# Kernel tuning notes

Measured on AMD Instinct MI355X. Metric: run time of the kernel, lower is better.

The kernel has to match this reference:

```python
import jax, jax.numpy as jnp
import numpy as np
from jax import lax

B, H, W = 2, 128, 128
DIM, HEADS, WS, SHIFT = 192, 6, 16, 8
NT, RD, CS, HID, K = 128, 20, 256, 384, 5
N = H * W
HD = DIM // HEADS


def _rpi(ws):
    coords = np.stack(np.meshgrid(np.arange(ws), np.arange(ws), indexing='ij')).reshape(2, -1)
    rel = (coords[:, :, None] - coords[:, None, :]).transpose(1, 2, 0).astype(np.int64)
    rel[:, :, 0] += ws - 1
    rel[:, :, 1] += ws - 1
    rel[:, :, 0] *= 2 * ws - 1
    return rel.sum(-1)


def _attn_mask(h, w, ws, shift):
    img = np.zeros((h, w))
    cnt = 0
    for hs in (slice(0, -ws), slice(-ws, -shift), slice(-shift, None)):
        for wsl in (slice(0, -ws), slice(-ws, -shift), slice(-shift, None)):
            img[hs, wsl] = cnt
            cnt += 1
    mw = img.reshape(h // ws, ws, w // ws, ws).transpose(0, 2, 1, 3).reshape(-1, ws * ws)
    am = mw[:, None, :] - mw[:, :, None]
    return np.where(am != 0, -100.0, 0.0).astype(np.float32)


def setup_inputs():
    key = jax.random.key(0)
    ks = jax.random.split(key, 16)
    f32 = jnp.float32
    rn = lambda k, shp, s=0.02: jax.random.normal(k, shp, dtype=f32) * s
    return {
        'x': jax.random.normal(ks[0], (B, N, DIM), dtype=f32),
        'td': jax.random.normal(ks[1], (B, NT, DIM), dtype=f32),
        'attn_mask': jnp.asarray(_attn_mask(H, W, WS, SHIFT)),
        'wqkv_w': rn(ks[2], (DIM, 3 * DIM)), 'wqkv_b': jnp.zeros((3 * DIM,), f32),
        'rpb_table': rn(ks[3], ((2 * WS - 1) ** 2, HEADS)),
        'win_proj_w': rn(ks[4], (DIM, DIM)), 'win_proj_b': jnp.zeros((DIM,), f32),
        'wq_w': rn(ks[5], (DIM, RD)), 'wq_b': jnp.zeros((RD,), f32),
        'wk_w': rn(ks[6], (DIM, RD)), 'wk_b': jnp.zeros((RD,), f32),
        'wv_w': rn(ks[7], (DIM, DIM)), 'wv_b': jnp.zeros((DIM,), f32),
        'atd_scale': jnp.full((NT,), 0.5, f32),
        'aca_proj_w': rn(ks[8], (DIM, DIM)), 'aca_proj_b': jnp.zeros((DIM,), f32),
        'logit_scale': jnp.full((1, 1), float(np.log(10.0)), f32),
        'fc1_w': rn(ks[9], (DIM, HID)), 'fc1_b': jnp.zeros((HID,), f32),
        'dw_w': rn(ks[10], (HID, 1, K, K)), 'dw_b': jnp.zeros((HID,), f32),
        'fc2_w': rn(ks[11], (HID, DIM)), 'fc2_b': jnp.zeros((DIM,), f32),
        'ln1_w': jnp.ones((DIM,), f32), 'ln1_b': jnp.zeros((DIM,), f32),
        'ln2_w': jnp.ones((DIM,), f32), 'ln2_b': jnp.zeros((DIM,), f32),
        'in3_w': jnp.ones((NT,), f32), 'in3_b': jnp.zeros((NT,), f32),
        'sigma': jnp.zeros((NT, 1), f32),
        'rpi': jnp.asarray(_rpi(WS)),
        'h': H, 'w': W,
    }


def _ln(x, w, b, eps=1e-5):
    mu = x.mean(-1, keepdims=True)
    var = ((x - mu) ** 2).mean(-1, keepdims=True)
    return (x - mu) * lax.rsqrt(var + eps) * w + b


def reference(x, td, attn_mask, wqkv_w, wqkv_b, rpb_table, win_proj_w, win_proj_b,
              wq_w, wq_b, wk_w, wk_b, wv_w, wv_b, atd_scale, aca_proj_w, aca_proj_b,
              logit_scale, fc1_w, fc1_b, dw_w, dw_b, fc2_w, fc2_b,
              ln1_w, ln1_b, ln2_w, ln2_b, in3_w, in3_b, sigma, rpi, h, w):
    b, n, c = x.shape
    shortcut = x
    xn = _ln(x, ln1_w, ln1_b)
    qkv = xn @ wqkv_w + wqkv_b  # (b, n, 3c)

    # ---- shifted-window MSA ----
    g = jnp.roll(qkv.reshape(b, h, w, 3 * c), (-SHIFT, -SHIFT), axis=(1, 2))
    nwh, nww = h // WS, w // WS
    nw2 = WS * WS
    win = g.reshape(b, nwh, WS, nww, WS, 3 * c).transpose(0, 1, 3, 2, 4, 5)
    win = win.reshape(b * nwh * nww, nw2, 3, HEADS, HD)
    q, k, v = (win[:, :, i].transpose(0, 2, 1, 3) for i in range(3))  # (b_, H, nw2, hd)
    attn = jnp.einsum('bhid,bhjd->bhij', q * (HD ** -0.5), k)
    rpb = rpb_table[rpi.reshape(-1)].reshape(nw2, nw2, HEADS).transpose(2, 0, 1)
    nwin = nwh * nww
    attn = attn.reshape(b, nwin, HEADS, nw2, nw2) + rpb[None, None] + attn_mask[None, :, None]
    attn = jax.nn.softmax(attn, axis=-1).reshape(-1, HEADS, nw2, nw2)
    o = jnp.einsum('bhij,bhjd->bhid', attn, v).transpose(0, 2, 1, 3).reshape(-1, nw2, c)
    o = o @ win_proj_w + win_proj_b
    o = o.reshape(b, nwh, nww, WS, WS, c).transpose(0, 1, 3, 2, 4, 5).reshape(b, h, w, c)
    x_win = jnp.roll(o, (SHIFT, SHIFT), axis=(1, 2)).reshape(b, n, c)

    # ---- adaptive token dictionary cross-attention ----
    qa = xn @ wq_w + wq_b
    ka = td @ wk_w + wk_b
    va = td @ wv_w + wv_b
    qa = qa / jnp.maximum(jnp.linalg.norm(qa, axis=-1, keepdims=True), 1e-12)
    ka = ka / jnp.maximum(jnp.linalg.norm(ka, axis=-1, keepdims=True), 1e-12)
    s = jnp.clip(atd_scale, 0.0, 1.0)
    sim = jax.nn.softmax(jnp.einsum('bnr,btr->bnt', qa, ka) * (1.0 + s * float(np.log(NT))), axis=-1)
    x_atd = jnp.einsum('bnt,btc->bnc', sim, va)

    # ---- adaptive category MSA (sort-gather-attend-scatter) ----
    gs = min(n, CS)
    ng = (n + gs - 1) // gs
    pad_n = ng * gs - n
    tk_id = jnp.argmax(sim, axis=-1)                      # (b, n)
    sort_idx = jnp.argsort(tk_id, axis=-1)
    inv_idx = jnp.argsort(sort_idx, axis=-1)              # inverse permutation
    shuf = jnp.take_along_axis(qkv, sort_idx[:, :, None], axis=1)
    if pad_n > 0:
        shuf = jnp.concatenate([shuf, shuf[:, n - pad_n:n][:, ::-1]], axis=1)
    y = shuf.reshape(b, ng, gs, 3, HEADS, HD)
    qg, kg, vg = (y[:, :, :, i].transpose(0, 1, 3, 2, 4) for i in range(3))  # (b, ng, H, gs, hd)
    ls = jnp.exp(jnp.minimum(logit_scale, float(np.log(100.0))))[0, 0]
    ag = jax.nn.softmax(jnp.einsum('bghid,bghjd->bghij', qg, kg) * ls, axis=-1)
    og = jnp.einsum('bghij,bghjd->bghid', ag, vg).transpose(0, 1, 3, 2, 4).reshape(b, ng * gs, c)[:, :n]
    og = jnp.take_along_axis(og, inv_idx[:, :, None], axis=1)
    x_aca = og @ aca_proj_w + aca_proj_b

    x = shortcut + x_win + x_atd + x_aca

    # ---- ConvFFN ----
    xn2 = _ln(x, ln2_w, ln2_b)
    hdn = jax.nn.gelu(xn2 @ fc1_w + fc1_b, approximate=False)
    grid = hdn.transpose(0, 2, 1).reshape(b, HID, h, w)
    grid = lax.conv_general_dilated(grid, dw_w, (1, 1), [(K // 2, K // 2)] * 2,
                                    feature_group_count=HID)
    grid = jax.nn.gelu(grid + dw_b[None, :, None, None], approximate=False)
    x = x + (grid.reshape(b, HID, n).transpose(0, 2, 1) @ fc2_w + fc2_b)

    # ---- token dictionary refinement ----
    mask_soft = jax.nn.softmax(jnp.swapaxes(sim, -1, -2), axis=-1)  # (b, NT, n)
    td_new = sigma * td + (1.0 - sigma) * jnp.einsum('btn,bnc->btc', mask_soft, x)
    mu = td_new.mean(-1, keepdims=True)
    var = ((td_new - mu) ** 2).mean(-1, keepdims=True)
    td_new = (td_new - mu) * lax.rsqrt(var + 1e-5) * in3_w[None, :, None] + in3_b[None, :, None]

    return x, td_new
```

## Files before the change

kernel.cpp:

```cpp
#include <hip/hip_runtime.h>
#include <math.h>

#define NB    2
#define HH    128
#define WW2   128
#define NN    16384
#define DIM_  192
#define HEADS_ 6
#define HD_   32
#define NT_   128
#define RD_   20
#define HID_  384
#define ROWS  32768
#define HD_SCALE 0.17677669529663687f
#define LOG100   4.6051701859880914f
#define LOGNT    4.852030263919617f

__device__ __forceinline__ float gelu_f(float v) {
  return 0.5f * v * (1.0f + erff(v * 0.7071067811865475f));
}

__device__ __forceinline__ int winmap_row(int r) {
  int b_ = r >> 8;
  int p  = r & 255;
  int b  = b_ >> 6;
  int win = b_ & 63;
  int y = ((win >> 3) << 4) + (p >> 4);
  int x = ((win & 7) << 4) + (p & 15);
  int n = (((y + 8) & 127) << 7) + ((x + 8) & 127);
  return (b << 14) + n;
}

__device__ __forceinline__ int rgn(int v) { return (v >= 112 ? 1 : 0) + (v >= 120 ? 1 : 0); }

__global__ __launch_bounds__(256)
void ln_kernel(const float* __restrict__ in, const float* __restrict__ w,
               const float* __restrict__ bv, float* __restrict__ out, int nrows) {
  int wave = threadIdx.x >> 6, lane = threadIdx.x & 63;
  int row = blockIdx.x * 4 + wave;
  if (row >= nrows) return;
  const float* p = in + (size_t)row * DIM_;
  float v0 = p[lane], v1 = p[lane + 64], v2 = p[lane + 128];
  float s = v0 + v1 + v2;
  #pragma unroll
  for (int m = 32; m; m >>= 1) s += __shfl_xor(s, m, 64);
  float mu = s * (1.0f / 192.0f);
  float d0 = v0 - mu, d1 = v1 - mu, d2 = v2 - mu;
  float q = d0 * d0 + d1 * d1 + d2 * d2;
  #pragma unroll
  for (int m = 32; m; m >>= 1) q += __shfl_xor(q, m, 64);
  float rs = rsqrtf(q * (1.0f / 192.0f) + 1e-5f);
  float* o = out + (size_t)row * DIM_;
  o[lane]       = d0 * rs * w[lane]       + bv[lane];
  o[lane + 64]  = d1 * rs * w[lane + 64]  + bv[lane + 64];
  o[lane + 128] = d2 * rs * w[lane + 128] + bv[lane + 128];
}

template<bool AT, bool BIAS, bool DOGELU, int RMODE, bool ADD>
__global__ __launch_bounds__(256)
void gemm128(const float* __restrict__ A, const float* __restrict__ W,
             const float* __restrict__ bias, float* __restrict__ C,
             int M, int N, int K, int lda, const int* __restrict__ rowmap) {
  __shared__ float As[32][128];
  __shared__ float Bs[32][64];
  int tid = threadIdx.x;
  int tx = tid & 15, ty = tid >> 4;
  int m0 = blockIdx.y * 128, n0 = blockIdx.x * 64;
  float acc[8][4] = {};
  for (int k0 = 0; k0 < K; k0 += 32) {
    if (!AT) {
      #pragma unroll
      for (int q = 0; q < 4; ++q) {
        int i = tid * 4 + q;
        int r = i >> 3, c4 = (i & 7) << 2;
        float4 v = *(const float4*)(A + (size_t)(m0 + r) * lda + k0 + c4);
        As[c4 + 0][r] = v.x; As[c4 + 1][r] = v.y; As[c4 + 2][r] = v.z; As[c4 + 3][r] = v.w;
      }
    } else {
      #pragma unroll
      for (int q = 0; q < 4; ++q) {
        int i = q * 256 + tid;
        int kc = i >> 5, mr4 = (i & 31) << 2;
        float4 v = *(const float4*)(A + (size_t)(k0 + kc) * lda + m0 + mr4);
        *(float4*)&As[kc][mr4] = v;
      }
    }
    #pragma unroll
    for (int q = 0; q < 2; ++q) {
      int i = tid * 2 + q;
      int kc = i >> 4, nc = (i & 15) << 2;
      int col = n0 + nc;
      float4 v = make_float4(0.f, 0.f, 0.f, 0.f);
      if (col + 3 < N) {
        v = *(const float4*)(W + (size_t)(k0 + kc) * N + col);
      } else {
        float t[4] = {0.f, 0.f, 0.f, 0.f};
        #pragma unroll
        for (int e = 0; e < 4; ++e) if (col + e < N) t[e] = W[(size_t)(k0 + kc) * N + col + e];
        v = make_float4(t[0], t[1], t[2], t[3]);
      }
      *(float4*)&Bs[kc][nc] = v;
    }
    __syncthreads();
    #pragma unroll
    for (int kk = 0; kk < 32; ++kk) {
      float4 a0 = *(const float4*)&As[kk][ty * 8];
      float4 a1 = *(const float4*)&As[kk][ty * 8 + 4];
      float4 b  = *(const float4*)&Bs[kk][tx * 4];
      float av[8] = {a0.x, a0.y, a0.z, a0.w, a1.x, a1.y, a1.z, a1.w};
      #pragma unroll
      for (int ii = 0; ii < 8; ++ii) {
        acc[ii][0] += av[ii] * b.x; acc[ii][1] += av[ii] * b.y;
        acc[ii][2] += av[ii] * b.z; acc[ii][3] += av[ii] * b.w;
      }
    }
    __syncthreads();
  }
  #pragma unroll
  for (int ii = 0; ii < 8; ++ii) {
    int row = m0 + ty * 8 + ii;
    int drow;
    if (RMODE == 1) drow = winmap_row(row);
    else if (RMODE == 2) drow = rowmap[row];
    else drow = row;
    float* crow = C + (size_t)drow * N;
    #pragma unroll
    for (int j = 0; j < 4; ++j) {
      int col = n0 + tx * 4 + j;
      if (col < N) {
        float v = acc[ii][j];
        if (BIAS) v += bias[col];
        if (DOGELU) v = gelu_f(v);
        if (ADD) crow[col] += v; else crow[col] = v;
      }
    }
  }
}

__global__ __launch_bounds__(256)
void attn2_kernel(const float* __restrict__ qkv, const int* __restrict__ sort_row,
                  const float* __restrict__ rpb_table, const float* __restrict__ ls_ptr,
                  float* __restrict__ obufW, float* __restrict__ obufC) {
  __shared__ float Ks[128][32];
  __shared__ float Vs[128][32];
  __shared__ float rpb_s[964];
  int b_ = blockIdx.x, head = blockIdx.y;
  bool IS_WIN = (blockIdx.z == 0);
  int tid = threadIdx.x;

  if (IS_WIN) {
    for (int idx = tid; idx < 961; idx += 256) rpb_s[idx] = rpb_table[idx * HEADS_ + head];
  }

  int gq = b_ * 256 + tid;
  int srcq = IS_WIN ? winmap_row(gq) : sort_row[gq];
  float qr[32];
  {
    const float4* rowp = (const float4*)(qkv + (size_t)srcq * 576);
    #pragma unroll
    for (int q4 = 0; q4 < 8; ++q4) {
      float4 v = rowp[head * 8 + q4];
      qr[q4 * 4] = v.x; qr[q4 * 4 + 1] = v.y; qr[q4 * 4 + 2] = v.z; qr[q4 * 4 + 3] = v.w;
    }
  }
  float scale = IS_WIN ? HD_SCALE : __expf(fminf(ls_ptr[0], LOG100));

  int win = b_ & 63;
  int wy = (win >> 3) << 4, wx = (win & 7) << 4;
  int py = tid >> 4, px = tid & 15;
  int ri = rgn(wy + py) * 3 + rgn(wx + px);

  float m = -3.4e38f, l = 0.f, acc[32];
  #pragma unroll
  for (int d = 0; d < 32; ++d) acc[d] = 0.f;

  for (int c0 = 0; c0 < 256; c0 += 128) {
    __syncthreads();
    #pragma unroll
    for (int it = 0; it < 4; ++it) {
      int j = it * 32 + (tid >> 3);
      int q4 = tid & 7;
      int src = IS_WIN ? winmap_row(b_ * 256 + c0 + j) : sort_row[b_ * 256 + c0 + j];
      const float4* rowp = (const float4*)(qkv + (size_t)src * 576);
      *(float4*)&Ks[j][q4 << 2] = rowp[48 + head * 8 + q4];
      *(float4*)&Vs[j][q4 << 2] = rowp[96 + head * 8 + q4];
    }
    __syncthreads();

    for (int j0 = 0; j0 < 128; j0 += 16) {
      float s[16];
      #pragma unroll
      for (int jj = 0; jj < 16; ++jj) {
        const float* kp = Ks[j0 + jj];
        float4 k0v = *(const float4*)(kp + 0),  k1v = *(const float4*)(kp + 4);
        float4 k2v = *(const float4*)(kp + 8),  k3v = *(const float4*)(kp + 12);
        float4 k4v = *(const float4*)(kp + 16), k5v = *(const float4*)(kp + 20);
        float4 k6v = *(const float4*)(kp + 24), k7v = *(const float4*)(kp + 28);
        float a = qr[0]*k0v.x + qr[1]*k0v.y + qr[2]*k0v.z + qr[3]*k0v.w
                + qr[4]*k1v.x + qr[5]*k1v.y + qr[6]*k1v.z + qr[7]*k1v.w
                + qr[8]*k2v.x + qr[9]*k2v.y + qr[10]*k2v.z + qr[11]*k2v.w
                + qr[12]*k3v.x + qr[13]*k3v.y + qr[14]*k3v.z + qr[15]*k3v.w
                + qr[16]*k4v.x + qr[17]*k4v.y + qr[18]*k4v.z + qr[19]*k4v.w
                + qr[20]*k5v.x + qr[21]*k5v.y + qr[22]*k5v.z + qr[23]*k5v.w
                + qr[24]*k6v.x + qr[25]*k6v.y + qr[26]*k6v.z + qr[27]*k6v.w
                + qr[28]*k7v.x + qr[29]*k7v.y + qr[30]*k7v.z + qr[31]*k7v.w;
        a *= scale;
        if (IS_WIN) {
          int jab = c0 + j0 + jj;
          int jy = jab >> 4, jx = jab & 15;
          int idx = (py - jy + 15) * 31 + (px - jx + 15);
          int rj = rgn(wy + jy) * 3 + rgn(wx + jx);
          a += rpb_s[idx] + (ri != rj ? -100.0f : 0.0f);
        }
        s[jj] = a;
      }
      float cm = s[0];
      #pragma unroll
      for (int jj = 1; jj < 16; ++jj) cm = fmaxf(cm, s[jj]);
      float mn = fmaxf(m, cm);
      float corr = __expf(m - mn);
      l *= corr;
      #pragma unroll
      for (int d = 0; d < 32; ++d) acc[d] *= corr;
      #pragma unroll
      for (int jj = 0; jj < 16; ++jj) {
        float p = __expf(s[jj] - mn);
        l += p;
        const float* vp = Vs[j0 + jj];
        #pragma unroll
        for (int d = 0; d < 32; ++d) acc[d] += p * vp[d];
      }
      m = mn;
    }
  }
  float inv = 1.0f / l;
  float* obuf = IS_WIN ? obufW : obufC;
  float* op = obuf + ((size_t)(b_ * 256 + tid)) * DIM_ + head * HD_;
  #pragma unroll
  for (int d4 = 0; d4 < 8; ++d4) {
    float4 v = make_float4(acc[d4 * 4] * inv, acc[d4 * 4 + 1] * inv,
                           acc[d4 * 4 + 2] * inv, acc[d4 * 4 + 3] * inv);
    *(float4*)(op + d4 * 4) = v;
  }
}

__global__ __launch_bounds__(256)
void normrows20(float* __restrict__ p, int rows) {
  int r = blockIdx.x * 256 + threadIdx.x;
  if (r >= rows) return;
  float4* rp = (float4*)(p + (size_t)r * RD_);
  float4 v[5];
  float s = 0.f;
  #pragma unroll
  for (int e = 0; e < 5; ++e) {
    v[e] = rp[e];
    s += v[e].x * v[e].x + v[e].y * v[e].y + v[e].z * v[e].z + v[e].w * v[e].w;
  }
  float inv = 1.0f / fmaxf(sqrtf(s), 1e-12f);
  #pragma unroll
  for (int e = 0; e < 5; ++e) {
    v[e].x *= inv; v[e].y *= inv; v[e].z *= inv; v[e].w *= inv;
    rp[e] = v[e];
  }
}

__global__ __launch_bounds__(256)
void sim1_kernel(const float* __restrict__ qa, const float* __restrict__ ka,
                 const float* __restrict__ atd_scale, float* __restrict__ simT,
                 float* __restrict__ m_out, float* __restrict__ den_out, int* __restrict__ tk) {
  __shared__ float kas[NT_ * RD_];
  __shared__ float scl[NT_];
  int tid = threadIdx.x;
  int gi = blockIdx.x * 256 + tid;
  int b = blockIdx.x >> 6;
  for (int idx = tid; idx < NT_ * RD_; idx += 256) kas[idx] = ka[b * NT_ * RD_ + idx];
  for (int t = tid; t < NT_; t += 256)
    scl[t] = 1.0f + fminf(fmaxf(atd_scale[t], 0.f), 1.f) * LOGNT;
  __syncthreads();
  float q[20];
  const float4* qp = (const float4*)(qa + (size_t)gi * RD_);
  #pragma unroll
  for (int e = 0; e < 5; ++e) {
    float4 v = qp[e];
    q[e * 4] = v.x; q[e * 4 + 1] = v.y; q[e * 4 + 2] = v.z; q[e * 4 + 3] = v.w;
  }
  int n = gi & (NN - 1);
  float m = -3.4e38f, l = 0.f;
  int am = 0;
  float* srow = simT + (size_t)b * NT_ * NN + n;
  for (int t = 0; t < NT_; ++t) {
    const float* kp = &kas[t * RD_];
    float d = 0.f;
    #pragma unroll
    for (int e = 0; e < 20; ++e) d += q[e] * kp[e];
    d *= scl[t];
    srow[(size_t)t * NN] = d;
    if (d > m) { l = l * __expf(m - d) + 1.0f; m = d; am = t; }
    else       { l += __expf(d - m); }
  }
  m_out[gi] = m; den_out[gi] = l; tk[gi] = am;
}

__global__ __launch_bounds__(256)
void sim2_kernel(float* __restrict__ simT, const float* __restrict__ m_i,
                 const float* __restrict__ den_i) {
  size_t idx = (size_t)blockIdx.x * 256 + threadIdx.x;
  int b = (int)(idx >> 21);
  int n = (int)(idx & (NN - 1));
  int gi = (b << 14) + n;
  float r = simT[idx];
  simT[idx] = __expf(r - m_i[gi]) / den_i[gi];
}

__global__ __launch_bounds__(256)
void hist_kernel(const int* __restrict__ tk, int* __restrict__ chist) {
  __shared__ int h[NT_];
  int tid = threadIdx.x, ch = blockIdx.x, b = blockIdx.y;
  if (tid < NT_) h[tid] = 0;
  __syncthreads();
  int bin = tk[b * NN + ch * 256 + tid];
  atomicAdd(&h[bin], 1);
  __syncthreads();
  if (tid < NT_) chist[(b * 64 + ch) * NT_ + tid] = h[tid];
}

__global__ __launch_bounds__(128)
void offsets_kernel(const int* __restrict__ chist, int* __restrict__ offs) {
  int b = blockIdx.x, bin = threadIdx.x;
  int total = 0;
  for (int ch = 0; ch < 64; ++ch) total += chist[(b * 64 + ch) * NT_ + bin];
  __shared__ int sc[NT_];
  sc[bin] = total;
  __syncthreads();
  int base = 0;
  for (int i = 0; i < bin; ++i) base += sc[i];
  int run = base;
  for (int ch = 0; ch < 64; ++ch) {
    offs[(b * 64 + ch) * NT_ + bin] = run;
    run += chist[(b * 64 + ch) * NT_ + bin];
  }
}

__global__ __launch_bounds__(256)
void scatter_kernel(const int* __restrict__ tk, const int* __restrict__ offs,
                    int* __restrict__ sort_row) {
  __shared__ int bins[256];
  int tid = threadIdx.x, ch = blockIdx.x, b = blockIdx.y;
  int i = ch * 256 + tid;
  int bin = tk[b * NN + i];
  bins[tid] = bin;
  __syncthreads();
  int rank = 0;
  for (int j = 0; j < tid; ++j) rank += (bins[j] == bin) ? 1 : 0;
  int pos = offs[(b * 64 + ch) * NT_ + bin] + rank;
  sort_row[b * NN + pos] = b * NN + i;
}

__global__ __launch_bounds__(384)
void dwconv_kernel(const float* __restrict__ hdn, const float* __restrict__ wgt,
                   const float* __restrict__ bv, float* __restrict__ out) {
  int c = threadIdx.x;
  int xt = blockIdx.x, y = blockIdx.y, b = blockIdx.z;
  float wr[25];
  #pragma unroll
  for (int t = 0; t < 25; ++t) wr[t] = wgt[c * 25 + t];
  float bias = bv[c];
  int x0 = xt * 16;
  const float* base = hdn + (size_t)b * NN * HID_;
  float win[5][5];
  #pragma unroll
  for (int r = 0; r < 5; ++r) {
    int yy = y + r - 2;
    #pragma unroll
    for (int t = 0; t < 4; ++t) {
      int xx = x0 - 2 + t;
      win[r][t] = (yy >= 0 && yy < HH && xx >= 0 && xx < WW2)
                    ? base[((size_t)yy * WW2 + xx) * HID_ + c] : 0.f;
    }
  }
  for (int x = x0; x < x0 + 16; ++x) {
    int xx = x + 2;
    #pragma unroll
    for (int r = 0; r < 5; ++r) {
      int yy = y + r - 2;
      win[r][4] = (yy >= 0 && yy < HH && xx < WW2)
                    ? base[((size_t)yy * WW2 + xx) * HID_ + c] : 0.f;
    }
    float s = bias;
    #pragma unroll
    for (int r = 0; r < 5; ++r)
      #pragma unroll
      for (int t = 0; t < 5; ++t) s += win[r][t] * wr[r * 5 + t];
    s = gelu_f(s);
    out[((size_t)b * NN + (size_t)y * WW2 + x) * HID_ + c] = s;
    #pragma unroll
    for (int r = 0; r < 5; ++r) {
      win[r][0] = win[r][1]; win[r][1] = win[r][2];
      win[r][2] = win[r][3]; win[r][3] = win[r][4];
    }
  }
}

__global__ __launch_bounds__(256)
void tdstats_kernel(const float* __restrict__ simT, float* __restrict__ tmax,
                    float* __restrict__ tden) {
  int bt = blockIdx.x;
  int tid = threadIdx.x;
  const float* row = simT + (size_t)bt * NN;
  float m = -3.4e38f;
  for (int i = tid; i < NN; i += 256) m = fmaxf(m, row[i]);
  __shared__ float red[256];
  red[tid] = m;
  __syncthreads();
  for (int s = 128; s > 0; s >>= 1) {
    if (tid < s) red[tid] = fmaxf(red[tid], red[tid + s]);
    __syncthreads();
  }
  float mrow = red[0];
  __syncthreads();
  float ssum = 0.f;
  for (int i = tid; i < NN; i += 256) ssum += __expf(row[i] - mrow);
  red[tid] = ssum;
  __syncthreads();
  for (int s = 128; s > 0; s >>= 1) {
    if (tid < s) red[tid] += red[tid + s];
    __syncthreads();
  }
  if (tid == 0) { tmax[bt] = mrow; tden[bt] = red[0]; }
}

__global__ __launch_bounds__(192)
void tdgemm_kernel(const float* __restrict__ simT, const float* __restrict__ tmax,
                   const float* __restrict__ tden, const float* __restrict__ xf,
                   float* __restrict__ tdacc) {
  int nch = blockIdx.x, tt4 = blockIdx.y, b = blockIdx.z;
  int t0 = tt4 * 32;
  int n0 = nch * 512;
  __shared__ float wtile[32][64];
  float acc[32] = {};
  int tid = threadIdx.x;
  for (int sub = 0; sub < 8; ++sub) {
    int nb = n0 + sub * 64;
    __syncthreads();
    for (int idx = tid; idx < 2048; idx += 192) {
      int trow = idx >> 6, nn = idx & 63;
      int t = t0 + trow;
      float raw = simT[((size_t)(b * NT_ + t)) * NN + nb + nn];
      wtile[trow][nn] = __expf(raw - tmax[b * NT_ + t]) / tden[b * NT_ + t];
    }
    __syncthreads();
    for (int nn = 0; nn < 64; ++nn) {
      float xv = xf[((size_t)(b * NN + nb + nn)) * DIM_ + tid];
      #pragma unroll
      for (int trow = 0; trow < 32; ++trow) acc[trow] += wtile[trow][nn] * xv;
    }
  }
  #pragma unroll
  for (int trow = 0; trow < 32; ++trow)
    atomicAdd(&tdacc[((size_t)(b * NT_ + t0 + trow)) * DIM_ + tid], acc[trow]);
}

__global__ __launch_bounds__(64)
void tdfinal_kernel(const float* __restrict__ td, const float* __restrict__ tdacc,
                    const float* __restrict__ sigma, const float* __restrict__ in3w,
                    const float* __restrict__ in3b, float* __restrict__ out) {
  int r = blockIdx.x;
  int lane = threadIdx.x;
  int t = r & (NT_ - 1);
  float sg = sigma[t];
  const float* ta = tdacc + (size_t)r * DIM_;
  const float* tp = td + (size_t)r * DIM_;
  float v0 = sg * tp[lane]       + (1.f - sg) * ta[lane];
  float v1 = sg * tp[lane + 64]  + (1.f - sg) * ta[lane + 64];
  float v2 = sg * tp[lane + 128] + (1.f - sg) * ta[lane + 128];
  float s = v0 + v1 + v2;
  #pragma unroll
  for (int m = 32; m; m >>= 1) s += __shfl_xor(s, m, 64);
  float mu = s * (1.0f / 192.0f);
  float d0 = v0 - mu, d1 = v1 - mu, d2 = v2 - mu;
  float q = d0 * d0 + d1 * d1 + d2 * d2;
  #pragma unroll
// ... 15 lines not shown
  const float* wqkv_w     = (const float*)d_in[3];
  const float* wqkv_b     = (const float*)d_in[4];
  const float* rpb_table  = (const float*)d_in[5];
  const float* win_proj_w = (const float*)d_in[6];
  const float* win_proj_b = (const float*)d_in[7];
  const float* wq_w       = (const float*)d_in[8];
  const float* wq_b       = (const float*)d_in[9];
  const float* wk_w       = (const float*)d_in[10];
  const float* wk_b       = (const float*)d_in[11];
  const float* wv_w       = (const float*)d_in[12];
  const float* wv_b       = (const float*)d_in[13];
  const float* atd_scale  = (const float*)d_in[14];
  const float* aca_proj_w = (const float*)d_in[15];
  const float* aca_proj_b = (const float*)d_in[16];
  const float* logit_scale= (const float*)d_in[17];
  const float* fc1_w      = (const float*)d_in[18];
  const float* fc1_b      = (const float*)d_in[19];
  const float* dw_w       = (const float*)d_in[20];
  const float* dw_b       = (const float*)d_in[21];
  const float* fc2_w      = (const float*)d_in[22];
  const float* fc2_b      = (const float*)d_in[23];
  const float* ln1_w      = (const float*)d_in[24];
  const float* ln1_b      = (const float*)d_in[25];
  const float* ln2_w      = (const float*)d_in[26];
  const float* ln2_b      = (const float*)d_in[27];
  const float* in3_w      = (const float*)d_in[28];
  const float* in3_b      = (const float*)d_in[29];
  const float* sigma      = (const float*)d_in[30];

  float* out = (float*)d_out;

  float* wsf = (float*)d_ws;
  size_t o = 0;
  float* xn    = wsf + o; o += (size_t)ROWS * DIM_;
  float* qkv   = wsf + o; o += (size_t)ROWS * 3 * DIM_;
  float* obufW = wsf + o; o += (size_t)ROWS * DIM_;
  float* simT  = wsf + o; o += (size_t)NB * NT_ * NN;
  float* gridb = wsf + o; o += (size_t)ROWS * HID_;
  float* qa    = wsf + o; o += (size_t)ROWS * RD_;
  float* ka    = wsf + o; o += (size_t)NB * NT_ * RD_;
  float* va    = wsf + o; o += (size_t)NB * NT_ * DIM_;
  float* m_i   = wsf + o; o += ROWS;
  float* den_i = wsf + o; o += ROWS;
  float* tmaxb = wsf + o; o += NB * NT_;
  float* tdenb = wsf + o; o += NB * NT_;
  float* tdacc = wsf + o; o += (size_t)NB * NT_ * DIM_;
  int* tk      = (int*)(wsf + o); o += ROWS;
  int* chist   = (int*)(wsf + o); o += NB * 64 * NT_;
  int* coffs   = (int*)(wsf + o); o += NB * 64 * NT_;
  int* sort_row= (int*)(wsf + o); o += ROWS;
  float* hdn   = qkv;
  float* obufC = gridb;

  hipMemcpyAsync(out, x, (size_t)ROWS * DIM_ * sizeof(float),
                 hipMemcpyDeviceToDevice, stream);
  ln_kernel<<<ROWS / 4, 256, 0, stream>>>(x, ln1_w, ln1_b, xn, ROWS);
  gemm128<false, true, false, 0, false><<<dim3(9, ROWS / 128), 256, 0, stream>>>(
      xn, wqkv_w, wqkv_b, qkv, ROWS, 576, 192, 192, nullptr);
  gemm128<false, true, false, 0, false><<<dim3(1, ROWS / 128), 256, 0, stream>>>(
      xn, wq_w, wq_b, qa, ROWS, 20, 192, 192, nullptr);
  gemm128<false, true, false, 0, false><<<dim3(1, 2), 256, 0, stream>>>(
      td, wk_w, wk_b, ka, NB * NT_, 20, 192, 192, nullptr);
  gemm128<false, true, false, 0, false><<<dim3(3, 2), 256, 0, stream>>>(
      td, wv_w, wv_b, va, NB * NT_, 192, 192, 192, nullptr);
  normrows20<<<ROWS / 256, 256, 0, stream>>>(qa, ROWS);
  normrows20<<<1, 256, 0, stream>>>(ka, NB * NT_);
  sim1_kernel<<<ROWS / 256, 256, 0, stream>>>(qa, ka, atd_scale, simT, m_i, den_i, tk);
  sim2_kernel<<<(NB * NT_ * NN) / 256, 256, 0, stream>>>(simT, m_i, den_i);
  hist_kernel<<<dim3(64, NB), 256, 0, stream>>>(tk, chist);
  offsets_kernel<<<NB, 128, 0, stream>>>(chist, coffs);
  scatter_kernel<<<dim3(64, NB), 256, 0, stream>>>(tk, coffs, sort_row);
  attn2_kernel<<<dim3(128, 6, 2), 256, 0, stream>>>(
      qkv, sort_row, rpb_table, logit_scale, obufW, obufC);
  gemm128<false, true, false, 1, true><<<dim3(3, ROWS / 128), 256, 0, stream>>>(
      obufW, win_proj_w, win_proj_b, out, ROWS, 192, 192, 192, nullptr);
  gemm128<false, true, false, 2, true><<<dim3(3, ROWS / 128), 256, 0, stream>>>(
      obufC, aca_proj_w, aca_proj_b, out, ROWS, 192, 192, 192, sort_row);
  for (int b = 0; b < NB; ++b) {
    gemm128<true, false, false, 0, true><<<dim3(3, NN / 128), 256, 0, stream>>>(
        simT + (size_t)b * NT_ * NN, va + (size_t)b * NT_ * DIM_, nullptr,
        out + (size_t)b * NN * DIM_, NN, 192, 128, NN, nullptr);
  }
  ln_kernel<<<ROWS / 4, 256, 0, stream>>>(out, ln2_w, ln2_b, xn, ROWS);
  gemm128<false, true, true, 0, false><<<dim3(6, ROWS / 128), 256, 0, stream>>>(
      xn, fc1_w, fc1_b, hdn, ROWS, 384, 192, 192, nullptr);
  dwconv_kernel<<<dim3(8, 128, NB), 384, 0, stream>>>(hdn, dw_w, dw_b, gridb);
  gemm128<false, true, false, 0, true><<<dim3(3, ROWS / 128), 256, 0, stream>>>(
      gridb, fc2_w, fc2_b, out, ROWS, 192, 384, 384, nullptr);
  tdstats_kernel<<<NB * NT_, 256, 0, stream>>>(simT, tmaxb, tdenb);
  hipMemsetAsync(tdacc, 0, (size_t)NB * NT_ * DIM_ * sizeof(float), stream);
  tdgemm_kernel<<<dim3(32, 4, NB), 192, 0, stream>>>(simT, tmaxb, tdenb, out, tdacc);
  tdfinal_kernel<<<NB * NT_, 64, 0, stream>>>(td, tdacc, sigma, in3_w, in3_b, out);
}
```

Before: 1.286 ms.

## Move main GEMMs to bf16 MFMA and store intermediates in bf16

Adds a bf16 MFMA GEMM kernel that reads pre-transposed, bf16-cast weights, and uses it for the qkv, projection, fc1, fc2 and similarity-times-V GEMMs. Intermediates (normalized activations, qkv, attention outputs, the FFN hidden state, similarity probabilities) are stored as bf16 to halve their memory traffic. The similarity matrix is now kept token-major and normalized in a single pass, which removes the separate sim2 kernel. The td statistics are now computed with a two-stage online softmax. Weight transposes run on every call, and the bf16 storage loses precision compared with the fp32 reference.

Result: faster. 1.037 ms (-19.4%).

```diff
diff --git a/kernel.cpp b/kernel.cpp
--- a/kernel.cpp
+++ b/kernel.cpp
@@ -16,6 +16,19 @@
 #define LOG100   4.6051701859880914f
 #define LOGNT    4.852030263919617f
 
+typedef __attribute__((ext_vector_type(8))) short s16x8;
+typedef __attribute__((ext_vector_type(4))) float f32x4;
+
+__device__ __forceinline__ float b2f(short h) {
+  unsigned u = ((unsigned)(unsigned short)h) << 16;
+  return __builtin_bit_cast(float, u);
+}
+__device__ __forceinline__ short f2b(float f) {
+  unsigned u = __builtin_bit_cast(unsigned, f);
+  u += 0x7fffu + ((u >> 16) & 1u);
+  return (short)(u >> 16);
+}
+
 __device__ __forceinline__ float gelu_f(float v) {
   return 0.5f * v * (1.0f + erff(v * 0.7071067811865475f));
 }
@@ -35,7 +48,8 @@
 
 __global__ __launch_bounds__(256)
 void ln_kernel(const float* __restrict__ in, const float* __restrict__ w,
-               const float* __restrict__ bv, float* __restrict__ out, int nrows) {
+               const float* __restrict__ bv, float* __restrict__ out,
+               short* __restrict__ outh, int nrows) {
   int wave = threadIdx.x >> 6, lane = threadIdx.x & 63;
   int row = blockIdx.x * 4 + wave;
   if (row >= nrows) return;
@@ -50,17 +64,102 @@
   #pragma unroll
   for (int m = 32; m; m >>= 1) q += __shfl_xor(q, m, 64);
   float rs = rsqrtf(q * (1.0f / 192.0f) + 1e-5f);
+  float r0 = d0 * rs * w[lane]       + bv[lane];
+  float r1 = d1 * rs * w[lane + 64]  + bv[lane + 64];
+  float r2 = d2 * rs * w[lane + 128] + bv[lane + 128];
   float* o = out + (size_t)row * DIM_;
-  o[lane]       = d0 * rs * w[lane]       + bv[lane];
-  o[lane + 64]  = d1 * rs * w[lane + 64]  + bv[lane + 64];
-  o[lane + 128] = d2 * rs * w[lane + 128] + bv[lane + 128];
-}
-
-template<bool AT, bool BIAS, bool DOGELU, int RMODE, bool ADD>
+  o[lane] = r0; o[lane + 64] = r1; o[lane + 128] = r2;
+  short* oh = outh + (size_t)row * DIM_;
+  oh[lane] = f2b(r0); oh[lane + 64] = f2b(r1); oh[lane + 128] = f2b(r2);
+}
+
+__global__ __launch_bounds__(256)
+void transcast(const float* __restrict__ W, short* __restrict__ Wt, int K, int N) {
+  __shared__ float tile[32][33];
+  int bx = blockIdx.x * 32, by = blockIdx.y * 32;
+  int tx = threadIdx.x & 31, ty = threadIdx.x >> 5;
+  #pragma unroll
+  for (int j = 0; j < 32; j += 8)
+    tile[ty + j][tx] = W[(size_t)(by + ty + j) * N + bx + tx];
+  __syncthreads();
+  #pragma unroll
+  for (int j = 0; j < 32; j += 8)
+    Wt[(size_t)(bx + ty + j) * K + by + tx] = f2b(tile[tx][ty + j]);
+}
+
+template<int KSTEPS, bool BIAS, bool DOGELU, int RMODE, int OUTMODE>
+__global__ __launch_bounds__(256)
+void gemm_mfma(const short* __restrict__ Ah, const short* __restrict__ Wt,
+               const float* __restrict__ bias, float* __restrict__ C,
+               short* __restrict__ Ch, int N, const int* __restrict__ rowmap) {
+  constexpr int K = KSTEPS * 32;
+  __shared__ short Asm[128][40];
+  __shared__ short Bsm[64][40];
+  int tid = threadIdx.x;
+  int m0 = blockIdx.y * 128, n0 = blockIdx.x * 64;
+  int w = tid >> 6, lane = tid & 63;
+  int wm = w >> 1, wn = w & 1;
+  int g = lane >> 4, r16 = lane & 15;
+  f32x4 acc[4][2] = {};
+  int srow = tid >> 1, shalf = tid & 1;
+  const short* aptr = Ah + (size_t)(m0 + srow) * K + shalf * 16;
+  const short* bptr = Wt + (size_t)(n0 + (srow & 63)) * K + shalf * 16;
+  for (int ks = 0; ks < KSTEPS; ++ks) {
+    s16x8 a0 = *(const s16x8*)(aptr);
+    s16x8 a1 = *(const s16x8*)(aptr + 8);
+    aptr += 32;
+    *(s16x8*)&Asm[srow][shalf * 16]     = a0;
+    *(s16x8*)&Asm[srow][shalf * 16 + 8] = a1;
+    if (tid < 128) {
+      s16x8 b0 = *(const s16x8*)(bptr);
+      s16x8 b1 = *(const s16x8*)(bptr + 8);
+      *(s16x8*)&Bsm[srow][shalf * 16]     = b0;
+      *(s16x8*)&Bsm[srow][shalf * 16 + 8] = b1;
+    }
+    bptr += 32;
+    __syncthreads();
+    s16x8 af[4], bfr[2];
+    #pragma unroll
+    for (int mi = 0; mi < 4; ++mi)
+      af[mi] = *(const s16x8*)&Asm[wm * 64 + mi * 16 + r16][g * 8];
+    #pragma unroll
+    for (int ni = 0; ni < 2; ++ni)
+      bfr[ni] = *(const s16x8*)&Bsm[wn * 32 + ni * 16 + r16][g * 8];
+    #pragma unroll
+    for (int mi = 0; mi < 4; ++mi)
+      #pragma unroll
+      for (int ni = 0; ni < 2; ++ni)
+        acc[mi][ni] = __builtin_amdgcn_mfma_f32_16x16x32_bf16(af[mi], bfr[ni], acc[mi][ni], 0, 0, 0);
+    __syncthreads();
+  }
+  #pragma unroll
+  for (int mi = 0; mi < 4; ++mi) {
+    #pragma unroll
+    for (int i = 0; i < 4; ++i) {
+      int row = m0 + wm * 64 + mi * 16 + 4 * g + i;
+      int drow;
+      if (RMODE == 1) drow = winmap_row(row);
+      else if (RMODE == 2) drow = rowmap[row];
+      else drow = row;
+      #pragma unroll
+      for (int ni = 0; ni < 2; ++ni) {
+        int col = n0 + wn * 32 + ni * 16 + r16;
+        float v = acc[mi][ni][i];
+        if (BIAS) v += bias[col];
+        if (DOGELU) v = gelu_f(v);
+        if (OUTMODE == 0)      C[(size_t)drow * N + col] = v;
+        else if (OUTMODE == 1) C[(size_t)drow * N + col] += v;
+        else                   Ch[(size_t)drow * N + col] = f2b(v);
+      }
+    }
+  }
+}
+
+template<bool BIAS>
 __global__ __launch_bounds__(256)
 void gemm128(const float* __restrict__ A, const float* __restrict__ W,
              const float* __restrict__ bias, float* __restrict__ C,
-             int M, int N, int K, int lda, const int* __restrict__ rowmap) {
+             int M, int N, int K, int lda) {
   __shared__ float As[32][128];
   __shared__ float Bs[32][64];
   int tid = threadIdx.x;
@@ -68,22 +167,12 @@
   int m0 = blockIdx.y * 128, n0 = blockIdx.x * 64;
   float acc[8][4] = {};
   for (int k0 = 0; k0 < K; k0 += 32) {
-    if (!AT) {
-      #pragma unroll
-      for (int q = 0; q < 4; ++q) {
-        int i = tid * 4 + q;
-        int r = i >> 3, c4 = (i & 7) << 2;
-        float4 v = *(const float4*)(A + (size_t)(m0 + r) * lda + k0 + c4);
-        As[c4 + 0][r] = v.x; As[c4 + 1][r] = v.y; As[c4 + 2][r] = v.z; As[c4 + 3][r] = v.w;
-      }
-    } else {
-      #pragma unroll
-      for (int q = 0; q < 4; ++q) {
-        int i = q * 256 + tid;
-        int kc = i >> 5, mr4 = (i & 31) << 2;
-        float4 v = *(const float4*)(A + (size_t)(k0 + kc) * lda + m0 + mr4);
-        *(float4*)&As[kc][mr4] = v;
-      }
+    #pragma unroll
+    for (int q = 0; q < 4; ++q) {
+      int i = tid * 4 + q;
+      int r = i >> 3, c4 = (i & 7) << 2;
+      float4 v = *(const float4*)(A + (size_t)(m0 + r) * lda + k0 + c4);
+      As[c4 + 0][r] = v.x; As[c4 + 1][r] = v.y; As[c4 + 2][r] = v.z; As[c4 + 3][r] = v.w;
     }
     #pragma unroll
     for (int q = 0; q < 2; ++q) {
@@ -119,30 +208,25 @@
   #pragma unroll
   for (int ii = 0; ii < 8; ++ii) {
     int row = m0 + ty * 8 + ii;
-    int drow;
-    if (RMODE == 1) drow = winmap_row(row);
-    else if (RMODE == 2) drow = rowmap[row];
-    else drow = row;
-    float* crow = C + (size_t)drow * N;
+    float* crow = C + (size_t)row * N;
     #pragma unroll
     for (int j = 0; j < 4; ++j) {
       int col = n0 + tx * 4 + j;
       if (col < N) {
         float v = acc[ii][j];
         if (BIAS) v += bias[col];
-        if (DOGELU) v = gelu_f(v);
-        if (ADD) crow[col] += v; else crow[col] = v;
+        crow[col] = v;
       }
     }
   }
 }
 
 __global__ __launch_bounds__(256)
-void attn2_kernel(const float* __restrict__ qkv, const int* __restrict__ sort_row,
+void attn2_kernel(const short* __restrict__ qkvh, const int* __restrict__ sort_row,
                   const float* __restrict__ rpb_table, const float* __restrict__ ls_ptr,
-                  float* __restrict__ obufW, float* __restrict__ obufC) {
-  __shared__ float Ks[128][32];
-  __shared__ float Vs[128][32];
+                  short* __restrict__ obufW, short* __restrict__ obufC) {
+  __shared__ float Ks[128][36];
+  __shared__ float Vs[128][36];
   __shared__ float rpb_s[964];
   int b_ = blockIdx.x, head = blockIdx.y;
   bool IS_WIN = (blockIdx.z == 0);
@@ -156,11 +240,12 @@
   int srcq = IS_WIN ? winmap_row(gq) : sort_row[gq];
   float qr[32];
   {
-    const float4* rowp = (const float4*)(qkv + (size_t)srcq * 576);
-    #pragma unroll
-    for (int q4 = 0; q4 < 8; ++q4) {
-      float4 v = rowp[head * 8 + q4];
-      qr[q4 * 4] = v.x; qr[q4 * 4 + 1] = v.y; qr[q4 * 4 + 2] = v.z; qr[q4 * 4 + 3] = v.w;
+    const short* rowp = qkvh + (size_t)srcq * 576 + head * 32;
+    #pragma unroll
+    for (int q8 = 0; q8 < 4; ++q8) {
+      s16x8 v = *(const s16x8*)(rowp + q8 * 8);
+      #pragma unroll
+      for (int e = 0; e < 8; ++e) qr[q8 * 8 + e] = b2f(v[e]);
     }
   }
   float scale = IS_WIN ? HD_SCALE : __expf(fminf(ls_ptr[0], LOG100));
@@ -174,16 +259,25 @@
   #pragma unroll
   for (int d = 0; d < 32; ++d) acc[d] = 0.f;
 
+  int j = tid >> 1, half = tid & 1;
   for (int c0 = 0; c0 < 256; c0 += 128) {
     __syncthreads();
-    #pragma unroll
-    for (int it = 0; it < 4; ++it) {
-      int j = it * 32 + (tid >> 3);
-      int q4 = tid & 7;
+    {
       int src = IS_WIN ? winmap_row(b_ * 256 + c0 + j) : sort_row[b_ * 256 + c0 + j];
-      const float4* rowp = (const float4*)(qkv + (size_t)src * 576);
-      *(float4*)&Ks[j][q4 << 2] = rowp[48 + head * 8 + q4];
-      *(float4*)&Vs[j][q4 << 2] = rowp[96 + head * 8 + q4];
+      const short* rowp = qkvh + (size_t)src * 576;
+      const short* kp = rowp + 192 + head * 32 + half * 16;
+      const short* vp = rowp + 384 + head * 32 + half * 16;
+      s16x8 k0 = *(const s16x8*)(kp), k1 = *(const s16x8*)(kp + 8);
+      s16x8 v0 = *(const s16x8*)(vp), v1 = *(const s16x8*)(vp + 8);
+      float4 f;
+      f = make_float4(b2f(k0[0]), b2f(k0[1]), b2f(k0[2]), b2f(k0[3])); *(float4*)&Ks[j][half*16]      = f;
+      f = make_float4(b2f(k0[4]), b2f(k0[5]), b2f(k0[6]), b2f(k0[7])); *(float4*)&Ks[j][half*16 + 4]  = f;
+      f = make_float4(b2f(k1[0]), b2f(k1[1]), b2f(k1[2]), b2f(k1[3])); *(float4*)&Ks[j][half*16 + 8]  = f;
+      f = make_float4(b2f(k1[4]), b2f(k1[5]), b2f(k1[6]), b2f(k1[7])); *(float4*)&Ks[j][half*16 + 12] = f;
+      f = make_float4(b2f(v0[0]), b2f(v0[1]), b2f(v0[2]), b2f(v0[3])); *(float4*)&Vs[j][half*16]      = f;
+      f = make_float4(b2f(v0[4]), b2f(v0[5]), b2f(v0[6]), b2f(v0[7])); *(float4*)&Vs[j][half*16 + 4]  = f;
+      f = make_float4(b2f(v1[0]), b2f(v1[1]), b2f(v1[2]), b2f(v1[3])); *(float4*)&Vs[j][half*16 + 8]  = f;
+      f = make_float4(b2f(v1[4]), b2f(v1[5]), b2f(v1[6]), b2f(v1[7])); *(float4*)&Vs[j][half*16 + 12] = f;
     }
     __syncthreads();
 
@@ -234,13 +328,14 @@
     }
   }
   float inv = 1.0f / l;
-  float* obuf = IS_WIN ? obufW : obufC;
-  float* op = obuf + ((size_t)(b_ * 256 + tid)) * DIM_ + head * HD_;
-  #pragma unroll
-  for (int d4 = 0; d4 < 8; ++d4) {
-    float4 v = make_float4(acc[d4 * 4] * inv, acc[d4 * 4 + 1] * inv,
-                           acc[d4 * 4 + 2] * inv, acc[d4 * 4 + 3] * inv);
-    *(float4*)(op + d4 * 4) = v;
+  short* obuf = IS_WIN ? obufW : obufC;
+  short* op = obuf + ((size_t)(b_ * 256 + tid)) * DIM_ + head * HD_;
+  #pragma unroll
+  for (int d8 = 0; d8 < 4; ++d8) {
+    s16x8 v;
+    #pragma unroll
+    for (int e = 0; e < 8; ++e) v[e] = f2b(acc[d8 * 8 + e] * inv);
+    *(s16x8*)(op + d8 * 8) = v;
   }
 }
 
@@ -266,8 +361,8 @@
 
 __global__ __launch_bounds__(256)
 void sim1_kernel(const float* __restrict__ qa, const float* __restrict__ ka,
-                 const float* __restrict__ atd_scale, float* __restrict__ simT,
-                 float* __restrict__ m_out, float* __restrict__ den_out, int* __restrict__ tk) {
+                 const float* __restrict__ atd_scale, float* __restrict__ simNat,
+                 short* __restrict__ simh, int* __restrict__ tk) {
   __shared__ float kas[NT_ * RD_];
   __shared__ float scl[NT_];
   int tid = threadIdx.x;
@@ -284,32 +379,40 @@
     float4 v = qp[e];
     q[e * 4] = v.x; q[e * 4 + 1] = v.y; q[e * 4 + 2] = v.z; q[e * 4 + 3] = v.w;
   }
-  int n = gi & (NN - 1);
   float m = -3.4e38f, l = 0.f;
   int am = 0;
-  float* srow = simT + (size_t)b * NT_ * NN + n;
   for (int t = 0; t < NT_; ++t) {
     const float* kp = &kas[t * RD_];
     float d = 0.f;
     #pragma unroll
     for (int e = 0; e < 20; ++e) d += q[e] * kp[e];
     d *= scl[t];
-    srow[(size_t)t * NN] = d;
     if (d > m) { l = l * __expf(m - d) + 1.0f; m = d; am = t; }
     else       { l += __expf(d - m); }
   }
-  m_out[gi] = m; den_out[gi] = l; tk[gi] = am;
-}
-
-__global__ __launch_bounds__(256)
-void sim2_kernel(float* __restrict__ simT, const float* __restrict__ m_i,
-                 const float* __restrict__ den_i) {
-  size_t idx = (size_t)blockIdx.x * 256 + threadIdx.x;
-  int b = (int)(idx >> 21);
-  int n = (int)(idx & (NN - 1));
-  int gi = (b << 14) + n;
-  float r = simT[idx];
-  simT[idx] = __expf(r - m_i[gi]) / den_i[gi];
+  tk[gi] = am;
+  float invl = 1.0f / l;
+  float* so = simNat + (size_t)gi * NT_;
+  short* sh = simh  + (size_t)gi * NT_;
+  for (int t0 = 0; t0 < NT_; t0 += 8) {
+    float p8[8];
+    #pragma unroll
+    for (int u = 0; u < 8; ++u) {
+      int t = t0 + u;
+      const float* kp = &kas[t * RD_];
+      float d = 0.f;
+      #pragma unroll
+      for (int e = 0; e < 20; ++e) d += q[e] * kp[e];
+      d *= scl[t];
+      p8[u] = __expf(d - m) * invl;
+    }
+    *(float4*)(so + t0)     = make_float4(p8[0], p8[1], p8[2], p8[3]);
+    *(float4*)(so + t0 + 4) = make_float4(p8[4], p8[5], p8[6], p8[7]);
+    s16x8 h;
+    #pragma unroll
+    for (int u = 0; u < 8; ++u) h[u] = f2b(p8[u]);
+    *(s16x8*)(sh + t0) = h;
+  }
 }
 
 __global__ __launch_bounds__(256)
@@ -351,14 +454,14 @@
   bins[tid] = bin;
   __syncthreads();
   int rank = 0;
-  for (int j = 0; j < tid; ++j) rank += (bins[j] == bin) ? 1 : 0;
+  for (int jq = 0; jq < tid; ++jq) rank += (bins[jq] == bin) ? 1 : 0;
   int pos = offs[(b * 64 + ch) * NT_ + bin] + rank;
   sort_row[b * NN + pos] = b * NN + i;
 }
 
 __global__ __launch_bounds__(384)
-void dwconv_kernel(const float* __restrict__ hdn, const float* __restrict__ wgt,
-                   const float* __restrict__ bv, float* __restrict__ out) {
+void dwconv_kernel(const short* __restrict__ hdn, const float* __restrict__ wgt,
+                   const float* __restrict__ bv, short* __restrict__ out) {
   int c = threadIdx.x;
   int xt = blockIdx.x, y = blockIdx.y, b = blockIdx.z;
   float wr[25];
@@ -366,7 +469,7 @@
   for (int t = 0; t < 25; ++t) wr[t] = wgt[c * 25 + t];
   float bias = bv[c];
   int x0 = xt * 16;
-  const float* base = hdn + (size_t)b * NN * HID_;
+  const short* base = hdn + (size_t)b * NN * HID_;
   float win[5][5];
   #pragma unroll
   for (int r = 0; r < 5; ++r) {
@@ -375,7 +478,7 @@
     for (int t = 0; t < 4; ++t) {
       int xx = x0 - 2 + t;
       win[r][t] = (yy >= 0 && yy < HH && xx >= 0 && xx < WW2)
-                    ? base[((size_t)yy * WW2 + xx) * HID_ + c] : 0.f;
+                    ? b2f(base[((size_t)yy * WW2 + xx) * HID_ + c]) : 0.f;
     }
   }
   for (int x = x0; x < x0 + 16; ++x) {
@@ -384,7 +487,7 @@
     for (int r = 0; r < 5; ++r) {
       int yy = y + r - 2;
       win[r][4] = (yy >= 0 && yy < HH && xx < WW2)
-                    ? base[((size_t)yy * WW2 + xx) * HID_ + c] : 0.f;
+                    ? b2f(base[((size_t)yy * WW2 + xx) * HID_ + c]) : 0.f;
     }
     float s = bias;
     #pragma unroll
@@ -392,7 +495,7 @@
       #pragma unroll
       for (int t = 0; t < 5; ++t) s += win[r][t] * wr[r * 5 + t];
     s = gelu_f(s);
-    out[((size_t)b * NN + (size_t)y * WW2 + x) * HID_ + c] = s;
+    out[((size_t)b * NN + (size_t)y * WW2 + x) * HID_ + c] = f2b(s);
     #pragma unroll
     for (int r = 0; r < 5; ++r) {
       win[r][0] = win[r][1]; win[r][1] = win[r][2];
@@ -402,51 +505,66 @@
 }
 
 __global__ __launch_bounds__(256)
-void tdstats_kernel(const float* __restrict__ simT, float* __restrict__ tmax,
-                    float* __restrict__ tden) {
-  int bt = blockIdx.x;
-  int tid = threadIdx.x;
-  const float* row = simT + (size_t)bt * NN;
-  float m = -3.4e38f;
-  for (int i = tid; i < NN; i += 256) m = fmaxf(m, row[i]);
-  __shared__ float red[256];
-  red[tid] = m;
+void tdstats1(const float* __restrict__ simNat, float* __restrict__ tpart) {
+  int b = blockIdx.y, seg = blockIdx.x;
+  int t = threadIdx.x & 127, half = threadIdx.x >> 7;
+  float m = -3.4e38f, l = 0.f;
+  const float* base = simNat + ((size_t)b * NN + seg * 1024 + half) * NT_ + t;
+  for (int i = 0; i < 512; ++i) {
+    float v = base[(size_t)i * 2 * NT_];
+    if (v > m) { l = l * __expf(m - v) + 1.f; m = v; } else l += __expf(v - m);
+  }
+  __shared__ float sm[256], sl[256];
+  sm[threadIdx.x] = m; sl[threadIdx.x] = l;
   __syncthreads();
-  for (int s = 128; s > 0; s >>= 1) {
-    if (tid < s) red[tid] = fmaxf(red[tid], red[tid + s]);
-    __syncthreads();
-  }
-  float mrow = red[0];
-  __syncthreads();
-  float ssum = 0.f;
-  for (int i = tid; i < NN; i += 256) ssum += __expf(row[i] - mrow);
-  red[tid] = ssum;
-  __syncthreads();
-  for (int s = 128; s > 0; s >>= 1) {
-    if (tid < s) red[tid] += red[tid + s];
-    __syncthreads();
-  }
-  if (tid == 0) { tmax[bt] = mrow; tden[bt] = red[0]; }
+  if (half == 0) {
+    float m2 = sm[t + 128], l2 = sl[t + 128];
+    float M = fmaxf(m, m2);
+    float L = l * __expf(m - M) + l2 * __expf(m2 - M);
+    tpart[((size_t)(b * 16 + seg) * 128 + t) * 2]     = M;
+    tpart[((size_t)(b * 16 + seg) * 128 + t) * 2 + 1] = L;
+  }
+}
+
+__global__ __launch_bounds__(256)
+void tdstats2(const float* __restrict__ tpart, float* __restrict__ tmax,
+              float* __restrict__ tden) {
+  int bt = threadIdx.x;
+  int b = bt >> 7, t = bt & 127;
+  float M = -3.4e38f, L = 0.f;
+  for (int s = 0; s < 16; ++s) {
+    float m = tpart[((size_t)(b * 16 + s) * 128 + t) * 2];
+    float l = tpart[((size_t)(b * 16 + s) * 128 + t) * 2 + 1];
+    float Mn = fmaxf(M, m);
+    L = L * __expf(M - Mn) + l * __expf(m - Mn);
+    M = Mn;
+  }
+  tmax[bt] = M; tden[bt] = L;
 }
 
 __global__ __launch_bounds__(192)
-void tdgemm_kernel(const float* __restrict__ simT, const float* __restrict__ tmax,
+void tdgemm_kernel(const float* __restrict__ simNat, const float* __restrict__ tmax,
                    const float* __restrict__ tden, const float* __restrict__ xf,
                    float* __restrict__ tdacc) {
   int nch = blockIdx.x, tt4 = blockIdx.y, b = blockIdx.z;
   int t0 = tt4 * 32;
   int n0 = nch * 512;
-  __shared__ float wtile[32][64];
+  __shared__ float wtile[32][65];
+  __shared__ float tmx[32], tdv[32];
+  int tid = threadIdx.x;
+  if (tid < 32) {
+    tmx[tid] = tmax[b * NT_ + t0 + tid];
+    tdv[tid] = tden[b * NT_ + t0 + tid];
+  }
+  __syncthreads();
   float acc[32] = {};
-  int tid = threadIdx.x;
   for (int sub = 0; sub < 8; ++sub) {
     int nb = n0 + sub * 64;
     __syncthreads();
     for (int idx = tid; idx < 2048; idx += 192) {
-      int trow = idx >> 6, nn = idx & 63;
-      int t = t0 + trow;
-      float raw = simT[((size_t)(b * NT_ + t)) * NN + nb + nn];
-      wtile[trow][nn] = __expf(raw - tmax[b * NT_ + t]) / tden[b * NT_ + t];
+      int nn = idx >> 5, tt = idx & 31;
+      float raw = simNat[((size_t)(b * NN + nb + nn)) * NT_ + t0 + tt];
+      wtile[tt][nn] = __expf(raw - tmx[tt]) / tdv[tt];
     }
     __syncthreads();
     for (int nn = 0; nn < 64; ++nn) {
@@ -528,63 +646,74 @@
 
   float* wsf = (float*)d_ws;
   size_t o = 0;
-  float* xn    = wsf + o; o += (size_t)ROWS * DIM_;
-  float* qkv   = wsf + o; o += (size_t)ROWS * 3 * DIM_;
-  float* obufW = wsf + o; o += (size_t)ROWS * DIM_;
-  float* simT  = wsf + o; o += (size_t)NB * NT_ * NN;
-  float* gridb = wsf + o; o += (size_t)ROWS * HID_;
-  float* qa    = wsf + o; o += (size_t)ROWS * RD_;
-  float* ka    = wsf + o; o += (size_t)NB * NT_ * RD_;
-  float* va    = wsf + o; o += (size_t)NB * NT_ * DIM_;
-  float* m_i   = wsf + o; o += ROWS;
-  float* den_i = wsf + o; o += ROWS;
-  float* tmaxb = wsf + o; o += NB * NT_;
-  float* tdenb = wsf + o; o += NB * NT_;
-  float* tdacc = wsf + o; o += (size_t)NB * NT_ * DIM_;
-  int* tk      = (int*)(wsf + o); o += ROWS;
-  int* chist   = (int*)(wsf + o); o += NB * 64 * NT_;
-  int* coffs   = (int*)(wsf + o); o += NB * 64 * NT_;
-  int* sort_row= (int*)(wsf + o); o += ROWS;
-  float* hdn   = qkv;
-  float* obufC = gridb;
-
+  float* xn     = wsf + o; o += (size_t)ROWS * DIM_;
+  short* xnh    = (short*)(wsf + o); o += (size_t)ROWS * DIM_ / 2;
+  short* qkvh   = (short*)(wsf + o); o += (size_t)ROWS * 3 * DIM_ / 2;
+  short* obufWh = (short*)(wsf + o); o += (size_t)ROWS * DIM_ / 2;
+  short* obufCh = (short*)(wsf + o); o += (size_t)ROWS * DIM_ / 2;
+  float* simNat = wsf + o; o += (size_t)ROWS * NT_;
+  short* simh   = (short*)(wsf + o); o += (size_t)ROWS * NT_ / 2;
+  short* gridh  = (short*)(wsf + o); o += (size_t)ROWS * HID_ / 2;
+  float* qa     = wsf + o; o += (size_t)ROWS * RD_;
+  float* ka     = wsf + o; o += (size_t)NB * NT_ * RD_;
+  float* va     = wsf + o; o += (size_t)NB * NT_ * DIM_;
+  short* vat    = (short*)(wsf + o); o += (size_t)NB * NT_ * DIM_ / 2;
+  float* tpart  = wsf + o; o += (size_t)NB * 16 * NT_ * 2;
+  float* tmaxb  = wsf + o; o += NB * NT_;
+  float* tdenb  = wsf + o; o += NB * NT_;
+  float* tdacc  = wsf + o; o += (size_t)NB * NT_ * DIM_;
+  int* tk       = (int*)(wsf + o); o += ROWS;
+  int* chist    = (int*)(wsf + o); o += NB * 64 * NT_;
+  int* coffs    = (int*)(wsf + o); o += NB * 64 * NT_;
+  int* sort_row = (int*)(wsf + o); o += ROWS;
+  short* wqkvT  = (short*)(wsf + o); o += (size_t)DIM_ * 576 / 2;
+  short* winT   = (short*)(wsf + o); o += (size_t)DIM_ * DIM_ / 2;
+  short* acaT   = (short*)(wsf + o); o += (size_t)DIM_ * DIM_ / 2;
+  short* fc1T   = (short*)(wsf + o); o += (size_t)DIM_ * HID_ / 2;
+  short* fc2T   = (short*)(wsf + o); o += (size_t)HID_ * DIM_ / 2;
+  short* hdnh   = qkvh;
+
+  transcast<<<dim3(576/32, 192/32), 256, 0, stream>>>(wqkv_w, wqkvT, 192, 576);
+  transcast<<<dim3(192/32, 192/32), 256, 0, stream>>>(win_proj_w, winT, 192, 192);
+  transcast<<<dim3(192/32, 192/32), 256, 0, stream>>>(aca_proj_w, acaT, 192, 192);
+  transcast<<<dim3(384/32, 192/32), 256, 0, stream>>>(fc1_w, fc1T, 192, 384);
+  transcast<<<dim3(192/32, 384/32), 256, 0, stream>>>(fc2_w, fc2T, 384, 192);
   hipMemcpyAsync(out, x, (size_t)ROWS * DIM_ * sizeof(float),
                  hipMemcpyDeviceToDevice, stream);
-  ln_kernel<<<ROWS / 4, 256, 0, stream>>>(x, ln1_w, ln1_b, xn, ROWS);
-  gemm128<false, true, false, 0, false><<<dim3(9, ROWS / 128), 256, 0, stream>>>(
-      xn, wqkv_w, wqkv_b, qkv, ROWS, 576, 192, 192, nullptr);
-  gemm128<false, true, false, 0, false><<<dim3(1, ROWS / 128), 256, 0, stream>>>(
-      xn, wq_w, wq_b, qa, ROWS, 20, 192, 192, nullptr);
-  gemm128<false, true, false, 0, false><<<dim3(1, 2), 256, 0, stream>>>(
-      td, wk_w, wk_b, ka, NB * NT_, 20, 192, 192, nullptr);
-  gemm128<false, true, false, 0, false><<<dim3(3, 2), 256, 0, stream>>>(
-      td, wv_w, wv_b, va, NB * NT_, 192, 192, 192, nullptr);
+  ln_kernel<<<ROWS / 4, 256, 0, stream>>>(x, ln1_w, ln1_b, xn, xnh, ROWS);
+  gemm_mfma<6, true, false, 0, 2><<<dim3(9, ROWS/128), 256, 0, stream>>>(
+      xnh, wqkvT, wqkv_b, nullptr, qkvh, 576, nullptr);
+  gemm128<true><<<dim3(1, ROWS/128), 256, 0, stream>>>(xn, wq_w, wq_b, qa, ROWS, 20, 192, 192);
+  gemm128<true><<<dim3(1, 2), 256, 0, stream>>>(td, wk_w, wk_b, ka, NB*NT_, 20, 192, 192);
+  gemm128<true><<<dim3(3, 2), 256, 0, stream>>>(td, wv_w, wv_b, va, NB*NT_, 192, 192, 192);
   normrows20<<<ROWS / 256, 256, 0, stream>>>(qa, ROWS);
   normrows20<<<1, 256, 0, stream>>>(ka, NB * NT_);
-  sim1_kernel<<<ROWS / 256, 256, 0, stream>>>(qa, ka, atd_scale, simT, m_i, den_i, tk);
-  sim2_kernel<<<(NB * NT_ * NN) / 256, 256, 0, stream>>>(simT, m_i, den_i);
+  transcast<<<dim3(192/32, 128/32), 256, 0, stream>>>(va, vat, 128, 192);
+  transcast<<<dim3(192/32, 128/32), 256, 0, stream>>>(va + (size_t)NT_*DIM_, vat + (size_t)DIM_*NT_, 128, 192);
+  sim1_kernel<<<ROWS / 256, 256, 0, stream>>>(qa, ka, atd_scale, simNat, simh, tk);
   hist_kernel<<<dim3(64, NB), 256, 0, stream>>>(tk, chist);
   offsets_kernel<<<NB, 128, 0, stream>>>(chist, coffs);
   scatter_kernel<<<dim3(64, NB), 256, 0, stream>>>(tk, coffs, sort_row);
   attn2_kernel<<<dim3(128, 6, 2), 256, 0, stream>>>(
-      qkv, sort_row, rpb_table, logit_scale, obufW, obufC);
-  gemm128<false, true, false, 1, true><<<dim3(3, ROWS / 128), 256, 0, stream>>>(
-      obufW, win_proj_w, win_proj_b, out, ROWS, 192, 192, 192, nullptr);
-  gemm128<false, true, false, 2, true><<<dim3(3, ROWS / 128), 256, 0, stream>>>(
-      obufC, aca_proj_w, aca_proj_b, out, ROWS, 192, 192, 192, sort_row);
+      qkvh, sort_row, rpb_table, logit_scale, obufWh, obufCh);
+  gemm_mfma<6, true, false, 1, 1><<<dim3(3, ROWS/128), 256, 0, stream>>>(
+      obufWh, winT, win_proj_b, out, nullptr, 192, nullptr);
+  gemm_mfma<6, true, false, 2, 1><<<dim3(3, ROWS/128), 256, 0, stream>>>(
+      obufCh, acaT, aca_proj_b, out, nullptr, 192, sort_row);
   for (int b = 0; b < NB; ++b) {
-    gemm128<true, false, false, 0, true><<<dim3(3, NN / 128), 256, 0, stream>>>(
-        simT + (size_t)b * NT_ * NN, va + (size_t)b * NT_ * DIM_, nullptr,
-        out + (size_t)b * NN * DIM_, NN, 192, 128, NN, nullptr);
-  }
-  ln_kernel<<<ROWS / 4, 256, 0, stream>>>(out, ln2_w, ln2_b, xn, ROWS);
-  gemm128<false, true, true, 0, false><<<dim3(6, ROWS / 128), 256, 0, stream>>>(
-      xn, fc1_w, fc1_b, hdn, ROWS, 384, 192, 192, nullptr);
-  dwconv_kernel<<<dim3(8, 128, NB), 384, 0, stream>>>(hdn, dw_w, dw_b, gridb);
-  gemm128<false, true, false, 0, true><<<dim3(3, ROWS / 128), 256, 0, stream>>>(
-      gridb, fc2_w, fc2_b, out, ROWS, 192, 384, 384, nullptr);
-  tdstats_kernel<<<NB * NT_, 256, 0, stream>>>(simT, tmaxb, tdenb);
+    gemm_mfma<4, false, false, 0, 1><<<dim3(3, NN/128), 256, 0, stream>>>(
+        simh + (size_t)b * NN * NT_, vat + (size_t)b * DIM_ * NT_, nullptr,
+        out + (size_t)b * NN * DIM_, nullptr, 192, nullptr);
+  }
+  ln_kernel<<<ROWS / 4, 256, 0, stream>>>(out, ln2_w, ln2_b, xn, xnh, ROWS);
+  gemm_mfma<6, true, true, 0, 2><<<dim3(6, ROWS/128), 256, 0, stream>>>(
+      xnh, fc1T, fc1_b, nullptr, hdnh, 384, nullptr);
+  dwconv_kernel<<<dim3(8, 128, NB), 384, 0, stream>>>(hdnh, dw_w, dw_b, gridh);
+  gemm_mfma<12, true, false, 0, 1><<<dim3(3, ROWS/128), 256, 0, stream>>>(
+      gridh, fc2T, fc2_b, out, nullptr, 192, nullptr);
+  tdstats1<<<dim3(16, NB), 256, 0, stream>>>(simNat, tpart);
+  tdstats2<<<1, 256, 0, stream>>>(tpart, tmaxb, tdenb);
   hipMemsetAsync(tdacc, 0, (size_t)NB * NT_ * DIM_ * sizeof(float), stream);
-  tdgemm_kernel<<<dim3(32, 4, NB), 192, 0, stream>>>(simT, tmaxb, tdenb, out, tdacc);
+  tdgemm_kernel<<<dim3(32, 4, NB), 192, 0, stream>>>(simNat, tmaxb, tdenb, out, tdacc);
   tdfinal_kernel<<<NB * NT_, 64, 0, stream>>>(td, tdacc, sigma, in3_w, in3_b, out);
 }
```
